# Kernel tuning notes

Measured on AMD Instinct MI355X. Metric: run time of the kernel, lower is better.

The kernel has to match this reference:

```python
import jax, jax.numpy as jnp
import numpy as np

B, T, C, H = 2, 2048, 768, 12
D = C // H              # head_dim = 64
LOCAL_WINDOW = 256
LN_EPS = 1e-5


def _layernorm(x, w, b):
    mu = jnp.mean(x, axis=-1, keepdims=True)
    var = jnp.var(x, axis=-1, keepdims=True)
    return (x - mu) * jax.lax.rsqrt(var + LN_EPS) * w + b


def setup_inputs() -> dict:
    key = jax.random.key(0)
    ks = jax.random.split(key, 8)
    inp = {
        "x": jax.random.normal(ks[0], (B, T, C), dtype=jnp.float32),
        "mamba_raw": jax.random.normal(ks[1], (B, T, C), dtype=jnp.float32),
        # c_attn / c_proj per nn.init in __init__
        "c_attn_w": 0.02 * jax.random.normal(ks[2], (C, 3 * C), dtype=jnp.float32),
        "c_attn_b": jnp.zeros((3 * C,), dtype=jnp.float32),
        "c_proj_w": 0.02 * jax.random.normal(ks[3], (C, C), dtype=jnp.float32),
        "c_proj_b": jnp.zeros((C,), dtype=jnp.float32),
        "ln_w": jnp.ones((C,), dtype=jnp.float32),
        "ln_b": jnp.zeros((C,), dtype=jnp.float32),
        "mamba_scale": jnp.asarray(0.1, dtype=jnp.float32),
        "sel_w": 0.01 * jax.random.normal(ks[4], (C, 1), dtype=jnp.float32),
        "sel_b": jnp.zeros((1,), dtype=jnp.float32),
        "local_weight": jnp.asarray(0.5, dtype=jnp.float32),
        "global_weight": jnp.asarray(0.5, dtype=jnp.float32),
    }
    return inp


def reference(x, mamba_raw, c_attn_w, c_attn_b, c_proj_w, c_proj_b,
              ln_w, ln_b, mamba_scale, sel_w, sel_b, local_weight, global_weight):
    scale = D ** -0.5
    qkv = x @ c_attn_w + c_attn_b                       # (B,T,3C)
    q, k, v = jnp.split(qkv, 3, axis=-1)
    q = q.reshape(B, T, H, D)
    k = k.reshape(B, T, H, D)
    v = v.reshape(B, T, H, D)

    scores = jnp.einsum('bihd,bjhd->bhij', q, k) * scale  # (B,H,T,T)
    i = jnp.arange(T)[:, None]
    j = jnp.arange(T)[None, :]
    causal = j > i                                       # mask strictly-future keys
    neg_inf = jnp.asarray(-jnp.inf, dtype=scores.dtype)
    scores = jnp.where(causal, neg_inf, scores)

    # frozen mamba branch (mamba_raw is a constant activation)
    mamba_raw = jax.lax.stop_gradient(mamba_raw)
    mamba_scaled = mamba_scale * _layernorm(mamba_raw, ln_w, ln_b)   # (B,T,C)
    sel = jax.nn.sigmoid(mamba_scaled @ sel_w + sel_b)               # (B,T,1)
    sel = sel[:, None, :, 0][:, :, None, :]                          # (B,1,1,T) over keys

    attn_global = scores * (0.5 + 0.5 * sel)             # -inf stays -inf

    outside_local = j < jnp.maximum(i - LOCAL_WINDOW, 0)
    attn_local = jnp.where(outside_local, neg_inf, scores)

    w_l = jax.nn.sigmoid(local_weight)
    w_g = jax.nn.sigmoid(global_weight)
    w_sum = w_l + w_g
    w_l, w_g = w_l / w_sum, w_g / w_sum

    attn_combined = w_l * jax.nn.softmax(attn_local, axis=-1) \
                  + w_g * jax.nn.softmax(attn_global, axis=-1)

    out = jnp.einsum('bhij,bjhd->bihd', attn_combined, v).reshape(B, T, C)
    return out @ c_proj_w + c_proj_b
```

## Files before the change

kernel.cpp:

```cpp
#include <hip/hip_runtime.h>
#include <math.h>

#define Bsz 2
#define Tsz 2048
#define Csz 768
#define Hsz 12
#define C3  2304
#define WIN 256
#define LN_EPS 1e-5f

#define QSCALE 0.1803368801111137f

typedef short bf16x8 __attribute__((ext_vector_type(8)));
typedef float f32x4  __attribute__((ext_vector_type(4)));

__device__ __forceinline__ unsigned short f2b(float f) {
    unsigned int u = __float_as_uint(f);
    u = (u + 0x7fffu + ((u >> 16) & 1u)) >> 16;
    return (unsigned short)u;
}

__device__ __forceinline__ float fast_exp2(float x) {
    float r;
    asm("v_exp_f32 %0, %1" : "=v"(r) : "v"(x));
    return r;
}

__global__ __launch_bounds__(256) void prep_fused(
    const float* __restrict__ x, unsigned short* __restrict__ xb,
    const float* __restrict__ c_attn_w, unsigned short* __restrict__ wq,
    const float* __restrict__ c_proj_w, unsigned short* __restrict__ wp,
    const float* __restrict__ mr, const float* __restrict__ ln_w,
    const float* __restrict__ ln_b, const float* __restrict__ scale_p,
    const float* __restrict__ sel_w, const float* __restrict__ sel_b,
    float* __restrict__ sel)
{
    __shared__ float tile[32][33];
    __shared__ float red1[256];
    __shared__ float red2[256];
    __shared__ float mu_sh, rstd_sh;

    const int blk = blockIdx.x;
    const int tid = threadIdx.x;

    if (blk < 3072) {
        int idx = blk * 256 + tid;
        float4 v = *(const float4*)(x + (size_t)idx * 4);
        unsigned int lo = (unsigned int)f2b(v.x) | ((unsigned int)f2b(v.y) << 16);
        unsigned int hi = (unsigned int)f2b(v.z) | ((unsigned int)f2b(v.w) << 16);
        uint2 o; o.x = lo; o.y = hi;
        *(uint2*)(xb + (size_t)idx * 4) = o;
        return;
    }
    if (blk < 5376) {
        const float* src; unsigned short* dst; int K, N, n0, k0;
        if (blk < 4800) {
            int i = blk - 3072;
            src = c_attn_w; dst = wq; K = Csz; N = C3;
            n0 = (i % 72) * 32; k0 = (i / 72) * 32;
        } else {
            int i = blk - 4800;
            src = c_proj_w; dst = wp; K = Csz; N = Csz;
            n0 = (i % 24) * 32; k0 = (i / 24) * 32;
        }
        const int tx = tid & 31, ty = tid >> 5;
        #pragma unroll
        for (int p = 0; p < 4; ++p)
            tile[ty + p * 8][tx] = src[(size_t)(k0 + ty + p * 8) * N + n0 + tx];
        __syncthreads();
        #pragma unroll
        for (int p = 0; p < 4; ++p)
            dst[(size_t)(n0 + ty + p * 8) * K + k0 + tx] = f2b(tile[tx][ty + p * 8]);
        return;
    }

    const int r = blk - 5376;
    const float* row = mr + (size_t)r * Csz;

    float s = 0.f, s2 = 0.f;
    for (int c = tid; c < Csz; c += 256) {
        float xv = row[c];
        s += xv; s2 += xv * xv;
    }
    red1[tid] = s; red2[tid] = s2;
    __syncthreads();
    for (int st = 128; st > 0; st >>= 1) {
        if (tid < st) { red1[tid] += red1[tid + st]; red2[tid] += red2[tid + st]; }
        __syncthreads();
    }
    if (tid == 0) {
        float mu = red1[0] * (1.f / Csz);
        float var = red2[0] * (1.f / Csz) - mu * mu;
        mu_sh = mu;
        rstd_sh = rsqrtf(var + LN_EPS);
    }
    __syncthreads();
    const float mu = mu_sh, rstd = rstd_sh;

    float dot = 0.f;
    for (int c = tid; c < Csz; c += 256) {
        float xn = (row[c] - mu) * rstd * ln_w[c] + ln_b[c];
        dot += xn * sel_w[c];
    }
    red1[tid] = dot;
    __syncthreads();
    for (int st = 128; st > 0; st >>= 1) {
        if (tid < st) red1[tid] += red1[tid + st];
        __syncthreads();
    }
    if (tid == 0) {
        float z = scale_p[0] * red1[0] + sel_b[0];
        sel[r] = 0.5f + 0.5f / (1.f + __expf(-z));
    }
}

template<int MODE>
__global__ __launch_bounds__(256) void gemm_bt_mfma(
    const unsigned short* __restrict__ A, const unsigned short* __restrict__ BT,
    const float* __restrict__ bias, void* __restrict__ Cout,
    unsigned short* __restrict__ KP, unsigned short* __restrict__ VP,
    int M, int N, int K)
{
    __shared__ unsigned short As[128 * 32];
    __shared__ unsigned short Bs[128 * 32];

    const int tid = threadIdx.x;
    const int lane = tid & 63, widx = tid >> 6;
    const int lm = lane & 15, quad = lane >> 4;
    const int wm = widx >> 1, wn = widx & 1;
    const int m0 = blockIdx.y * 128, n0 = blockIdx.x * 128;

    f32x4 acc[4][4];
    #pragma unroll
    for (int mt = 0; mt < 4; ++mt)
        #pragma unroll
        for (int nt = 0; nt < 4; ++nt)
            acc[mt][nt] = f32x4{0.f, 0.f, 0.f, 0.f};

    int rowS[2], cS[2];
    #pragma unroll
    for (int t = 0; t < 2; ++t) {
        int idx = t * 256 + tid;
        rowS[t] = idx >> 2;
        cS[t] = idx & 3;
    }

    bf16x8 pa[2], pb[2];
    #pragma unroll
    for (int t = 0; t < 2; ++t) {
        pa[t] = *(const bf16x8*)(A + (size_t)(m0 + rowS[t]) * K + cS[t] * 8);
        pb[t] = *(const bf16x8*)(BT + (size_t)(n0 + rowS[t]) * K + cS[t] * 8);
    }

    const int nk = K / 32;
    for (int kt = 0; kt < nk; ++kt) {
        __syncthreads();
        #pragma unroll
        for (int t = 0; t < 2; ++t) {
            *(bf16x8*)(&As[rowS[t] * 32 + ((cS[t] ^ ((rowS[t] >> 1) & 3)) << 3)]) = pa[t];
            *(bf16x8*)(&Bs[rowS[t] * 32 + ((cS[t] ^ ((rowS[t] >> 1) & 3)) << 3)]) = pb[t];
        }
        __syncthreads();
        if (kt + 1 < nk) {
            int k0 = (kt + 1) * 32;
            #pragma unroll
            for (int t = 0; t < 2; ++t) {
                pa[t] = *(const bf16x8*)(A + (size_t)(m0 + rowS[t]) * K + k0 + cS[t] * 8);
                pb[t] = *(const bf16x8*)(BT + (size_t)(n0 + rowS[t]) * K + k0 + cS[t] * 8);
            }
        }
        bf16x8 af[4], bf[4];
        #pragma unroll
        for (int mt = 0; mt < 4; ++mt) {
            int m = wm * 64 + mt * 16 + lm;
            af[mt] = *(const bf16x8*)(&As[m * 32 + ((quad ^ ((m >> 1) & 3)) << 3)]);
        }
        #pragma unroll
        for (int nt = 0; nt < 4; ++nt) {
            int n = wn * 64 + nt * 16 + lm;
            bf[nt] = *(const bf16x8*)(&Bs[n * 32 + ((quad ^ ((n >> 1) & 3)) << 3)]);
        }
        #pragma unroll
        for (int mt = 0; mt < 4; ++mt)
            #pragma unroll
            for (int nt = 0; nt < 4; ++nt)
                acc[mt][nt] = __builtin_amdgcn_mfma_f32_16x16x32_bf16(
                    af[mt], bf[nt], acc[mt][nt], 0, 0, 0);
    }

    float bv[4];
    #pragma unroll
    for (int nt = 0; nt < 4; ++nt)
        bv[nt] = bias[n0 + wn * 64 + nt * 16 + lm];

    #pragma unroll
    for (int mt = 0; mt < 4; ++mt) {
        #pragma unroll
        for (int nt = 0; nt < 4; ++nt) {
            const int cb = n0 + wn * 64 + nt * 16;
            const int col = cb + lm;
            const int rbase = m0 + wm * 64 + mt * 16 + quad * 4;
            if (MODE == 0) {
                #pragma unroll
                for (int r = 0; r < 4; ++r)
                    ((float*)Cout)[(size_t)(rbase + r) * N + col] =
                        acc[mt][nt][r] + bv[nt];
            } else if (cb < Csz) {
                #pragma unroll
                for (int r = 0; r < 4; ++r)
                    ((unsigned short*)Cout)[(size_t)(rbase + r) * Csz + col] =
                        f2b((acc[mt][nt][r] + bv[nt]) * QSCALE);
            } else if (cb < 2 * Csz) {
                const int dfull = col - Csz;
                const int h = dfull >> 6, dd = dfull & 63;
                const int f = dd >> 5, qd = (dd >> 3) & 3, j = dd & 7;
                #pragma unroll
                for (int r = 0; r < 4; ++r) {
                    const int row = rbase + r;
                    const int b = row >> 11, t = row & 2047;
                    const int ktk = t >> 4, lmk = t & 15;
                    size_t addr = ((((size_t)((b * Hsz + h) * 128 + ktk)) * 2 + f) * 512)
                                  + (qd * 16 + lmk) * 8 + j;
                    KP[addr] = f2b(acc[mt][nt][r] + bv[nt]);
                }
            } else {
                const int dfull = col - 2 * Csz;
                const int h = dfull >> 6, dd = dfull & 63;
                const int ntv = dd >> 4, lmv = dd & 15;
                #pragma unroll
                for (int r = 0; r < 4; ++r) {
                    const int row = rbase + r;
                    const int b = row >> 11, t = row & 2047;
                    const int jtv = t >> 5, qv = (t >> 3) & 3, j = t & 7;
                    size_t addr = (((size_t)((b * Hsz + h) * 64 + jtv) * 4 + ntv) * 512)
                                  + (qv * 16 + lmv) * 8 + j;
                    VP[addr] = f2b(acc[mt][nt][r] + bv[nt]);
                }
            }
        }
    }
}

__global__ __launch_bounds__(256) void attn_mfma(
    const unsigned short* __restrict__ qb, const unsigned short* __restrict__ KP,
    const unsigned short* __restrict__ VP, const float* __restrict__ fsel_arr,
    const float* __restrict__ lw_p, const float* __restrict__ gw_p,
    unsigned short* __restrict__ attnb)
{
    __shared__ __align__(16) unsigned char SMEM[36864];

    const int tid = threadIdx.x;
    const int widx = tid >> 6, lane = tid & 63;
    const int lm = lane & 15, quad = lane >> 4;

    unsigned short* Pb = (unsigned short*)SMEM + widx * 4 * (16 * 72);
    float* MrgF = (float*)SMEM;
    #define MRG(slot, br, row, col) MrgF[((((slot) * 2 + (br)) * 16 + (row)) * 66) + (col)]

    const int strip = 127 - (int)(blockIdx.x / 24);
    const int bh = (int)(blockIdx.x % 24);
    const int h = bh % Hsz, b = bh / Hsz;
    const int i0 = strip * 16;

    const unsigned short* KPb = KP + (size_t)bh * 131072 + lane * 8;
    const unsigned short* VPb = VP + (size_t)bh * 131072 + lane * 8;

    const unsigned short* qrow =
        qb + (size_t)(b * Tsz + i0 + lm) * Csz + h * 64 + quad * 8;
    const bf16x8 qf0 = *(const bf16x8*)qrow;
    const bf16x8 qf1 = *(const bf16x8*)(qrow + 32);

    float l_g[4], l_l[4];
    f32x4 Og[4], Ol[4];
    #pragma unroll
    for (int r = 0; r < 4; ++r) { l_g[r] = 0.f; l_l[r] = 0.f; }
    #pragma unroll
    for (int nt = 0; nt < 4; ++nt) {
        Og[nt] = f32x4{0.f, 0.f, 0.f, 0.f};
        Ol[nt] = f32x4{0.f, 0.f, 0.f, 0.f};
    }

    const int jtd = i0 >> 6;
    const int jtl = (jtd - 4) > 0 ? (jtd - 4) : 0;

    auto phaseA = [&](int jt, int slot) {
        const int j0 = jt * 64;
        const bool diag = (jt == jtd);
        const bool firstloc = (jt == jtl) && !diag;
        const bool loc = (jt >= jtl);
        unsigned short* Pg = Pb + (slot * 2 + 0) * (16 * 72);
        unsigned short* Pl = Pb + (slot * 2 + 1) * (16 * 72);

        const unsigned short* kp = KPb + (size_t)(j0 >> 4) * 1024;
        f32x4 s[4];
        #pragma unroll
        for (int nt = 0; nt < 4; ++nt) {
            bf16x8 k0 = *(const bf16x8*)(kp + nt * 1024);
            bf16x8 k1 = *(const bf16x8*)(kp + nt * 1024 + 512);
            f32x4 z = f32x4{0.f, 0.f, 0.f, 0.f};
            z = __builtin_amdgcn_mfma_f32_16x16x32_bf16(qf0, k0, z, 0, 0, 0);
            z = __builtin_amdgcn_mfma_f32_16x16x32_bf16(qf1, k1, z, 0, 0, 0);
            s[nt] = z;
        }

        float fs[4];
        #pragma unroll
        for (int nt = 0; nt < 4; ++nt)
            fs[nt] = fsel_arr[b * Tsz + j0 + nt * 16 + lm];

        if (diag) {
            #pragma unroll
            for (int r = 0; r < 4; ++r) {
                const int qi = i0 + quad * 4 + r;
                #pragma unroll
                for (int nt = 0; nt < 4; ++nt) {
                    const int kj = j0 + nt * 16 + lm;
                    float p = fast_exp2(s[nt][r] * fs[nt]);
                    p = (kj > qi) ? 0.f : p;
                    unsigned int u = __float_as_uint(p);
                    l_g[r] += __uint_as_float(u & 0xffff0000u);
                    Pg[(quad * 4 + r) * 72 + nt * 16 + lm] = (unsigned short)(u >> 16);
                }
            }
        } else {
            #pragma unroll
            for (int r = 0; r < 4; ++r)
                #pragma unroll
                for (int nt = 0; nt < 4; ++nt) {
                    float p = fast_exp2(s[nt][r] * fs[nt]);
                    unsigned int u = __float_as_uint(p);
                    l_g[r] += __uint_as_float(u & 0xffff0000u);
                    Pg[(quad * 4 + r) * 72 + nt * 16 + lm] = (unsigned short)(u >> 16);
                }
        }

        if (loc) {
            if (diag) {
                #pragma unroll
                for (int r = 0; r < 4; ++r) {
                    const int qi = i0 + quad * 4 + r;
                    #pragma unroll
                    for (int nt = 0; nt < 4; ++nt) {
                        const int kj = j0 + nt * 16 + lm;
                        float p = fast_exp2(s[nt][r]);
                        p = (kj > qi || kj < qi - WIN) ? 0.f : p;
                        unsigned int u = __float_as_uint(p);
                        l_l[r] += __uint_as_float(u & 0xffff0000u);
                        Pl[(quad * 4 + r) * 72 + nt * 16 + lm] = (unsigned short)(u >> 16);
                    }
                }
            } else if (firstloc) {
                #pragma unroll
                for (int r = 0; r < 4; ++r) {
                    const int qi = i0 + quad * 4 + r;
                    #pragma unroll
                    for (int nt = 0; nt < 4; ++nt) {
                        const int kj = j0 + nt * 16 + lm;
                        float p = fast_exp2(s[nt][r]);
                        p = (kj < qi - WIN) ? 0.f : p;
                        unsigned int u = __float_as_uint(p);
                        l_l[r] += __uint_as_float(u & 0xffff0000u);
                        Pl[(quad * 4 + r) * 72 + nt * 16 + lm] = (unsigned short)(u >> 16);
                    }
                }
            } else {
                #pragma unroll
                for (int r = 0; r < 4; ++r)
                    #pragma unroll
                    for (int nt = 0; nt < 4; ++nt) {
                        float p = fast_exp2(s[nt][r]);
                        unsigned int u = __float_as_uint(p);
                        l_l[r] += __uint_as_float(u & 0xffff0000u);
                        Pl[(quad * 4 + r) * 72 + nt * 16 + lm] = (unsigned short)(u >> 16);
                    }
            }
        }
    };

    auto phaseB = [&](int jt, int slot) {
        const int j0 = jt * 64;
        const bool loc = (jt >= jtl);
        unsigned short* Pg = Pb + (slot * 2 + 0) * (16 * 72);
        unsigned short* Pl = Pb + (slot * 2 + 1) * (16 * 72);

        const bf16x8 ag0 = *(const bf16x8*)(&Pg[lm * 72 + quad * 8]);
        const bf16x8 ag1 = *(const bf16x8*)(&Pg[lm * 72 + 32 + quad * 8]);
        bf16x8 al0 = {}, al1 = {};
        if (loc) {
            al0 = *(const bf16x8*)(&Pl[lm * 72 + quad * 8]);
            al1 = *(const bf16x8*)(&Pl[lm * 72 + 32 + quad * 8]);
        }

        const unsigned short* vp = VPb + (size_t)(j0 >> 5) * 2048;
        #pragma unroll
        for (int nt = 0; nt < 4; ++nt) {
            bf16x8 v0 = *(const bf16x8*)(vp + nt * 512);
            bf16x8 v1 = *(const bf16x8*)(vp + 2048 + nt * 512);
            Og[nt] = __builtin_amdgcn_mfma_f32_16x16x32_bf16(ag0, v0, Og[nt], 0, 0, 0);
            Og[nt] = __builtin_amdgcn_mfma_f32_16x16x32_bf16(ag1, v1, Og[nt], 0, 0, 0);
            if (loc) {
                Ol[nt] = __builtin_amdgcn_mfma_f32_16x16x32_bf16(al0, v0, Ol[nt], 0, 0, 0);
                Ol[nt] = __builtin_amdgcn_mfma_f32_16x16x32_bf16(al1, v1, Ol[nt], 0, 0, 0);
            }
        }
    };

    for (int jt = widx; jt <= jtd; jt += 8) {
        const int jt2 = jt + 4;
        const bool has2 = (jt2 <= jtd);
        phaseA(jt, 0);
        if (has2) phaseA(jt2, 1);
        phaseB(jt, 0);
        if (has2) phaseB(jt2, 1);
    }

    #pragma unroll
    for (int st = 1; st < 16; st <<= 1) {
        #pragma unroll
        for (int r = 0; r < 4; ++r) {
            l_g[r] += __shfl_xor(l_g[r], st);
            l_l[r] += __shfl_xor(l_l[r], st);
        }
    }

    auto write_slot = [&](int slot) {
        #pragma unroll
        for (int r = 0; r < 4; ++r) {
            const int row = quad * 4 + r;
            #pragma unroll
            for (int nt = 0; nt < 4; ++nt) {
                MRG(slot, 0, row, nt * 16 + lm) = Og[nt][r];
                MRG(slot, 1, row, nt * 16 + lm) = Ol[nt][r];
            }
            if (lm == 0) {
                MRG(slot, 0, row, 65) = l_g[r];
                MRG(slot, 1, row, 65) = l_l[r];
            }
        }
    };
    auto combine_slot = [&](int slot) {
        #pragma unroll
        for (int r = 0; r < 4; ++r) {
            const int row = quad * 4 + r;
            {
                l_g[r] += MRG(slot, 0, row, 65);
                #pragma unroll
                for (int nt = 0; nt < 4; ++nt)
                    Og[nt][r] += MRG(slot, 0, row, nt * 16 + lm);
            }
            {
                l_l[r] += MRG(slot, 1, row, 65);
                #pragma unroll
                for (int nt = 0; nt < 4; ++nt)
                    Ol[nt][r] += MRG(slot, 1, row, nt * 16 + lm);
            }
        }
    };

    __syncthreads();
    if (widx == 1) write_slot(0);
    if (widx == 3) write_slot(1);
    __syncthreads();
    if (widx == 0) combine_slot(0);
    if (widx == 2) combine_slot(1);
    __syncthreads();
    if (widx == 2) write_slot(0);
    __syncthreads();

    if (widx == 0) {
        combine_slot(0);

        float wl = 1.f / (1.f + __expf(-lw_p[0]));
        float wg = 1.f / (1.f + __expf(-gw_p[0]));
        float ws = wl + wg;
        wl /= ws; wg /= ws;

        #pragma unroll
        for (int r = 0; r < 4; ++r) {
            const int row = quad * 4 + r;
            const float cg = wg / l_g[r];
            const float cl = wl / l_l[r];
            #pragma unroll
            for (int nt = 0; nt < 4; ++nt) {
                float v = Og[nt][r] * cg + Ol[nt][r] * cl;
                attnb[(size_t)(b * Tsz + i0 + row) * Csz + h * 64 + nt * 16 + lm] =
                    f2b(v);
            }
        }
    }
    #undef MRG
}

extern "C" void kernel_launch(void* const* d_in, const int* in_sizes, int n_in,
                              void* d_out, int out_size, void* d_ws, size_t ws_size,
                              hipStream_t stream)
{
    const float* x          = (const float*)d_in[0];
    const float* mamba_raw  = (const float*)d_in[1];
    const float* c_attn_w   = (const float*)d_in[2];
    const float* c_attn_b   = (const float*)d_in[3];
    const float* c_proj_w   = (const float*)d_in[4];
    const float* c_proj_b   = (const float*)d_in[5];
    const float* ln_w       = (const float*)d_in[6];
    const float* ln_b       = (const float*)d_in[7];
    const float* mamba_sc   = (const float*)d_in[8];
    const float* sel_w      = (const float*)d_in[9];
    const float* sel_b      = (const float*)d_in[10];
    const float* local_w    = (const float*)d_in[11];
    const float* global_w   = (const float*)d_in[12];
    float* out = (float*)d_out;

    const int M = Bsz * Tsz;

    unsigned short* xb    = (unsigned short*)d_ws;
    unsigned short* wq    = xb + (size_t)M * Csz;
    unsigned short* wp    = wq + (size_t)C3 * Csz;
    unsigned short* qb    = wp + (size_t)Csz * Csz;
    unsigned short* kpb   = qb + (size_t)M * Csz;
    unsigned short* vpb   = kpb + (size_t)24 * 131072;
    unsigned short* attnb = vpb + (size_t)24 * 131072;
    float* sel = (float*)(attnb + (size_t)M * Csz);

    prep_fused<<<9472, 256, 0, stream>>>(x, xb, c_attn_w, wq, c_proj_w, wp,
                                         mamba_raw, ln_w, ln_b, mamba_sc,
                                         sel_w, sel_b, sel);

    {
        dim3 g(C3 / 128, M / 128);
        gemm_bt_mfma<1><<<g, 256, 0, stream>>>(xb, wq, c_attn_b, qb,
                                               kpb, vpb, M, C3, Csz);
    }

    attn_mfma<<<128 * Hsz * Bsz, 256, 0, stream>>>(qb, kpb, vpb, sel,
                                                   local_w, global_w, attnb);

    {
        dim3 g(Csz / 128, M / 128);
        gemm_bt_mfma<0><<<g, 256, 0, stream>>>(attnb, wp, c_proj_b, out,
                                               nullptr, nullptr, M, Csz, Csz);
    }
}
```

Measured before the change: 193.9 us.

## Compute softmax row sums via MFMA with ones vector, drop two-slot interleave

Row sums of the softmax probabilities are now computed by extra MFMAs that multiply the bf16 P tiles by a ones column, instead of per-element scalar accumulation followed by a cross-lane shuffle reduction. The previous two-tile interleaved loop (phaseA/phaseB over two slots) is collapsed into a single-tile loop per iteration, which halves the shared-memory P buffer. K fragments are loaded up front before the score MFMAs. This trades VALU adds and shuffles for extra matrix-core work, and gives up the explicit overlap between two tiles, which may reduce latency hiding.

```diff
diff --git a/kernel.cpp b/kernel.cpp
--- a/kernel.cpp
+++ b/kernel.cpp
@@ -247,13 +247,14 @@
     const float* __restrict__ lw_p, const float* __restrict__ gw_p,
     unsigned short* __restrict__ attnb)
 {
-    __shared__ __align__(16) unsigned char SMEM[36864];
+    __shared__ __align__(16) unsigned char SMEM[18432];
 
     const int tid = threadIdx.x;
     const int widx = tid >> 6, lane = tid & 63;
     const int lm = lane & 15, quad = lane >> 4;
 
-    unsigned short* Pb = (unsigned short*)SMEM + widx * 4 * (16 * 72);
+    unsigned short* Pg = (unsigned short*)SMEM + (widx * 2 + 0) * (16 * 72);
+    unsigned short* Pl = (unsigned short*)SMEM + (widx * 2 + 1) * (16 * 72);
     float* MrgF = (float*)SMEM;
     #define MRG(slot, br, row, col) MrgF[((((slot) * 2 + (br)) * 16 + (row)) * 66) + (col)]
 
@@ -270,36 +271,41 @@
     const bf16x8 qf0 = *(const bf16x8*)qrow;
     const bf16x8 qf1 = *(const bf16x8*)(qrow + 32);
 
-    float l_g[4], l_l[4];
-    f32x4 Og[4], Ol[4];
-    #pragma unroll
-    for (int r = 0; r < 4; ++r) { l_g[r] = 0.f; l_l[r] = 0.f; }
+    const short o1 = (lm == 0) ? (short)0x3F80 : (short)0;
+    const bf16x8 of = bf16x8{o1, o1, o1, o1, o1, o1, o1, o1};
+
+    f32x4 Og[4], Ol[4], lsg, lsl;
     #pragma unroll
     for (int nt = 0; nt < 4; ++nt) {
         Og[nt] = f32x4{0.f, 0.f, 0.f, 0.f};
         Ol[nt] = f32x4{0.f, 0.f, 0.f, 0.f};
     }
+    lsg = f32x4{0.f, 0.f, 0.f, 0.f};
+    lsl = f32x4{0.f, 0.f, 0.f, 0.f};
 
     const int jtd = i0 >> 6;
     const int jtl = (jtd - 4) > 0 ? (jtd - 4) : 0;
 
-    auto phaseA = [&](int jt, int slot) {
+    for (int jt = widx; jt <= jtd; jt += 4) {
         const int j0 = jt * 64;
         const bool diag = (jt == jtd);
         const bool firstloc = (jt == jtl) && !diag;
         const bool loc = (jt >= jtl);
-        unsigned short* Pg = Pb + (slot * 2 + 0) * (16 * 72);
-        unsigned short* Pl = Pb + (slot * 2 + 1) * (16 * 72);
 
         const unsigned short* kp = KPb + (size_t)(j0 >> 4) * 1024;
+        bf16x8 kc0[4], kc1[4];
+        #pragma unroll
+        for (int nt = 0; nt < 4; ++nt) {
+            kc0[nt] = *(const bf16x8*)(kp + nt * 1024);
+            kc1[nt] = *(const bf16x8*)(kp + nt * 1024 + 512);
+        }
+
         f32x4 s[4];
         #pragma unroll
         for (int nt = 0; nt < 4; ++nt) {
-            bf16x8 k0 = *(const bf16x8*)(kp + nt * 1024);
-            bf16x8 k1 = *(const bf16x8*)(kp + nt * 1024 + 512);
             f32x4 z = f32x4{0.f, 0.f, 0.f, 0.f};
-            z = __builtin_amdgcn_mfma_f32_16x16x32_bf16(qf0, k0, z, 0, 0, 0);
-            z = __builtin_amdgcn_mfma_f32_16x16x32_bf16(qf1, k1, z, 0, 0, 0);
+            z = __builtin_amdgcn_mfma_f32_16x16x32_bf16(qf0, kc0[nt], z, 0, 0, 0);
+            z = __builtin_amdgcn_mfma_f32_16x16x32_bf16(qf1, kc1[nt], z, 0, 0, 0);
             s[nt] = z;
         }
 
@@ -317,9 +323,8 @@
                     const int kj = j0 + nt * 16 + lm;
                     float p = fast_exp2(s[nt][r] * fs[nt]);
                     p = (kj > qi) ? 0.f : p;
-                    unsigned int u = __float_as_uint(p);
-                    l_g[r] += __uint_as_float(u & 0xffff0000u);
-                    Pg[(quad * 4 + r) * 72 + nt * 16 + lm] = (unsigned short)(u >> 16);
+                    Pg[(quad * 4 + r) * 72 + nt * 16 + lm] =
+                        (unsigned short)(__float_as_uint(p) >> 16);
                 }
             }
         } else {
@@ -328,9 +333,8 @@
                 #pragma unroll
                 for (int nt = 0; nt < 4; ++nt) {
                     float p = fast_exp2(s[nt][r] * fs[nt]);
-                    unsigned int u = __float_as_uint(p);
-                    l_g[r] += __uint_as_float(u & 0xffff0000u);
-                    Pg[(quad * 4 + r) * 72 + nt * 16 + lm] = (unsigned short)(u >> 16);
+                    Pg[(quad * 4 + r) * 72 + nt * 16 + lm] =
+                        (unsigned short)(__float_as_uint(p) >> 16);
                 }
         }
 
@@ -344,9 +348,8 @@
                         const int kj = j0 + nt * 16 + lm;
                         float p = fast_exp2(s[nt][r]);
                         p = (kj > qi || kj < qi - WIN) ? 0.f : p;
-                        unsigned int u = __float_as_uint(p);
-                        l_l[r] += __uint_as_float(u & 0xffff0000u);
-                        Pl[(quad * 4 + r) * 72 + nt * 16 + lm] = (unsigned short)(u >> 16);
+                        Pl[(quad * 4 + r) * 72 + nt * 16 + lm] =
+                            (unsigned short)(__float_as_uint(p) >> 16);
                     }
                 }
             } else if (firstloc) {
@@ -358,9 +361,8 @@
                         const int kj = j0 + nt * 16 + lm;
                         float p = fast_exp2(s[nt][r]);
                         p = (kj < qi - WIN) ? 0.f : p;
-                        unsigned int u = __float_as_uint(p);
-                        l_l[r] += __uint_as_float(u & 0xffff0000u);
-                        Pl[(quad * 4 + r) * 72 + nt * 16 + lm] = (unsigned short)(u >> 16);
+                        Pl[(quad * 4 + r) * 72 + nt * 16 + lm] =
+                            (unsigned short)(__float_as_uint(p) >> 16);
                     }
                 }
             } else {
@@ -369,19 +371,11 @@
                     #pragma unroll
                     for (int nt = 0; nt < 4; ++nt) {
                         float p = fast_exp2(s[nt][r]);
-                        unsigned int u = __float_as_uint(p);
-                        l_l[r] += __uint_as_float(u & 0xffff0000u);
-                        Pl[(quad * 4 + r) * 72 + nt * 16 + lm] = (unsigned short)(u >> 16);
+                        Pl[(quad * 4 + r) * 72 + nt * 16 + lm] =
+                            (unsigned short)(__float_as_uint(p) >> 16);
                     }
             }
         }
-    };
-
-    auto phaseB = [&](int jt, int slot) {
-        const int j0 = jt * 64;
-        const bool loc = (jt >= jtl);
-        unsigned short* Pg = Pb + (slot * 2 + 0) * (16 * 72);
-        unsigned short* Pl = Pb + (slot * 2 + 1) * (16 * 72);
 
         const bf16x8 ag0 = *(const bf16x8*)(&Pg[lm * 72 + quad * 8]);
         const bf16x8 ag1 = *(const bf16x8*)(&Pg[lm * 72 + 32 + quad * 8]);
@@ -389,6 +383,13 @@
         if (loc) {
             al0 = *(const bf16x8*)(&Pl[lm * 72 + quad * 8]);
             al1 = *(const bf16x8*)(&Pl[lm * 72 + 32 + quad * 8]);
+        }
+
+        lsg = __builtin_amdgcn_mfma_f32_16x16x32_bf16(ag0, of, lsg, 0, 0, 0);
+        lsg = __builtin_amdgcn_mfma_f32_16x16x32_bf16(ag1, of, lsg, 0, 0, 0);
+        if (loc) {
+            lsl = __builtin_amdgcn_mfma_f32_16x16x32_bf16(al0, of, lsl, 0, 0, 0);
+            lsl = __builtin_amdgcn_mfma_f32_16x16x32_bf16(al1, of, lsl, 0, 0, 0);
         }
 
         const unsigned short* vp = VPb + (size_t)(j0 >> 5) * 2048;
@@ -403,25 +404,11 @@
                 Ol[nt] = __builtin_amdgcn_mfma_f32_16x16x32_bf16(al1, v1, Ol[nt], 0, 0, 0);
             }
         }
-    };
-
-    for (int jt = widx; jt <= jtd; jt += 8) {
-        const int jt2 = jt + 4;
-        const bool has2 = (jt2 <= jtd);
-        phaseA(jt, 0);
-        if (has2) phaseA(jt2, 1);
-        phaseB(jt, 0);
-        if (has2) phaseB(jt2, 1);
-    }
-
-    #pragma unroll
-    for (int st = 1; st < 16; st <<= 1) {
-        #pragma unroll
-        for (int r = 0; r < 4; ++r) {
-            l_g[r] += __shfl_xor(l_g[r], st);
-            l_l[r] += __shfl_xor(l_l[r], st);
-        }
-    }
+    }
+
+    float l_g[4], l_l[4];
+    #pragma unroll
+    for (int r = 0; r < 4; ++r) { l_g[r] = lsg[r]; l_l[r] = lsl[r]; }
 
     auto write_slot = [&](int slot) {
         #pragma unroll
@@ -469,6 +456,12 @@
 
     if (widx == 0) {
         combine_slot(0);
+
+        #pragma unroll
+        for (int r = 0; r < 4; ++r) {
+            l_g[r] = __shfl(l_g[r], quad << 4);
+            l_l[r] = __shfl(l_l[r], quad << 4);
+        }
 
         float wl = 1.f / (1.f + __expf(-lw_p[0]));
         float wg = 1.f / (1.f + __expf(-gw_p[0]));
```

Measured after the change: 197.1 us. No clear change (+1.6%).
